# Kernel optimization log

Hardware: AMD Instinct MI355X
Metric: run time of the kernel (lower is better)

The kernel has to match this reference:

```python
import jax, jax.numpy as jnp
import numpy as np

N, E, G = 20000, 320000, 64
IN_CH, HID, HEADS = 128, 64, 8
LEAKY_SLOPE = 0.2
SOFTMAX_EPS = 1e-16


def setup_inputs() -> dict:
    key = jax.random.key(0)
    ks = jax.random.split(key, 12)
    s = lambda fan_in: 1.0 / np.sqrt(fan_in)
    return {
        "x": jax.random.normal(ks[0], (N, IN_CH), jnp.float32),
        "edge_index": jax.random.randint(ks[1], (2, E), 0, N, jnp.int32),
        "batch": jnp.sort(jax.random.randint(ks[2], (N,), 0, G, jnp.int32)),
        "W1": jax.random.normal(ks[3], (HEADS * HID, IN_CH), jnp.float32) * s(IN_CH),
        "att_src1": jax.random.normal(ks[4], (HEADS, HID), jnp.float32) * s(HID),
        "att_dst1": jax.random.normal(ks[5], (HEADS, HID), jnp.float32) * s(HID),
        "b1": jnp.zeros((HEADS * HID,), jnp.float32),
        "W2": jax.random.normal(ks[6], (HID, HEADS * HID), jnp.float32) * s(HEADS * HID),
        "att_src2": jax.random.normal(ks[7], (1, HID), jnp.float32) * s(HID),
        "att_dst2": jax.random.normal(ks[8], (1, HID), jnp.float32) * s(HID),
        "b2": jnp.zeros((HID,), jnp.float32),
    }


def gat_conv(x, src, dst, W, att_src, att_dst, b):
    # x: [N, F_in]; W: [H*C, F_in]; att_*: [H, C]; b: [H*C]
    n = x.shape[0]
    heads, ch = att_src.shape
    h = (x @ W.T).reshape(n, heads, ch)                    # [N,H,C]
    a_s = jnp.einsum('nhc,hc->nh', h, att_src)             # [N,H]
    a_d = jnp.einsum('nhc,hc->nh', h, att_dst)             # [N,H]
    e = jax.nn.leaky_relu(a_s[src] + a_d[dst], LEAKY_SLOPE)  # [E,H]
    m = jax.ops.segment_max(e, dst, num_segments=n)        # scatter-softmax (stable)
    e = jnp.exp(e - m[dst])
    z = jax.ops.segment_sum(e, dst, num_segments=n)
    alpha = e / (z[dst] + SOFTMAX_EPS)                     # [E,H]
    msg = h[src] * alpha[:, :, None]                       # [E,H,C]
    out = jax.ops.segment_sum(msg, dst, num_segments=n)    # [N,H,C]
    return out.reshape(n, heads * ch) + b


def reference(x, edge_index, batch, W1, att_src1, att_dst1, b1, W2, att_src2, att_dst2, b2):
    # PyG GATConv default: add self loops
    loop = jnp.arange(N, dtype=edge_index.dtype)
    src = jnp.concatenate([edge_index[0], loop])
    dst = jnp.concatenate([edge_index[1], loop])

    x_mid = jax.nn.relu(gat_conv(x, src, dst, W1, att_src1, att_dst1, b1))  # [N, H*C]

    # global_mean_pool over `batch` segments
    sums = jax.ops.segment_sum(x_mid, batch, num_segments=G)
    cnt = jax.ops.segment_sum(jnp.ones((N,), x_mid.dtype), batch, num_segments=G)
    gat_mid_pooled = sums / jnp.maximum(cnt, 1.0)[:, None]                  # [G, H*C]

    # dropout identity in eval mode
    x_late = gat_conv(x_mid, src, dst, W2, att_src2, att_dst2, b2)          # [N, C]
    gat_late_view = x_late.reshape(-1, HEADS * HID)                          # [N/H, H*C]
    return gat_mid_pooled, gat_late_view
```

## Files before the change

### kernel.cpp

```cpp
#include <hip/hip_runtime.h>
#include <math.h>

#define NN 20000
#define EE 320000
#define ETOT 340000
#define GG 64
#define INCH 128
#define HIDC 64
#define NH 8
#define HC 512
#define SLOPE 0.2f
#define SMEPS 1e-16f

typedef unsigned short u16;
typedef unsigned int u32;
typedef __attribute__((ext_vector_type(8))) short bf16x8;
typedef __attribute__((ext_vector_type(4))) float f32x4;

__device__ __forceinline__ float rlanef(float v, int l) {
  return __uint_as_float(__builtin_amdgcn_readlane(__float_as_uint(v), l));
}
__device__ __forceinline__ u16 f2bf(float f) {
  u32 x = __float_as_uint(f);
  x += 0x7FFFu + ((x >> 16) & 1u);
  return (u16)(x >> 16);
}

__global__ void k_hist(const int* __restrict__ ei, int* __restrict__ deg) {
  int i = blockIdx.x * 256 + threadIdx.x;
  if (i >= ETOT) return;
  int d = (i < EE) ? ei[EE + i] : (i - EE);
  atomicAdd(&deg[d], 1);
}

__global__ void k_scan(const int* __restrict__ deg, int* __restrict__ rowstart) {
  __shared__ int wsum[16];
  __shared__ int carry_sh;
  int tid = threadIdx.x;
  int lane = tid & 63, w = tid >> 6;
  if (tid == 0) { carry_sh = 0; rowstart[0] = 0; }
  __syncthreads();
  for (int base = 0; base < NN; base += 1024) {
    int v = (base + tid < NN) ? deg[base + tid] : 0;
    int s = v;
#pragma unroll
    for (int off = 1; off < 64; off <<= 1) {
      int t = __shfl_up(s, off);
      if (lane >= off) s += t;
    }
    if (lane == 63) wsum[w] = s;
    __syncthreads();
    if (w == 0 && lane < 16) {
      int t = wsum[lane];
#pragma unroll
      for (int off = 1; off < 16; off <<= 1) {
        int u = __shfl_up(t, off);
        if (lane >= off) t += u;
      }
      wsum[lane] = t;
    }
    __syncthreads();
    int waveoff = (w == 0) ? 0 : wsum[w - 1];
    int incl = s + waveoff + carry_sh;
    if (base + tid < NN) rowstart[base + tid + 1] = incl;
    __syncthreads();
    if (tid == 1023) carry_sh = incl;
    __syncthreads();
  }
}

__global__ void k_fill(const int* __restrict__ ei, const int* __restrict__ rowstart,
                       int* __restrict__ wcur, int* __restrict__ csr) {
  int i = blockIdx.x * 256 + threadIdx.x;
  if (i >= ETOT) return;
  int s, d;
  if (i < EE) { s = ei[i]; d = ei[EE + i]; } else { s = i - EE; d = s; }
  int pos = rowstart[d] + atomicAdd(&wcur[d], 1);
  csr[pos] = s;
}

__global__ void k_prep(const float* __restrict__ W1, const float* __restrict__ W2,
                       const float* __restrict__ as1, const float* __restrict__ ad1v,
                       u16* __restrict__ W1bf, u16* __restrict__ W2bf,
                       float* __restrict__ wB1) {
  int i = blockIdx.x * 256 + threadIdx.x;
  if (i < 65536) {
    W1bf[i] = f2bf(W1[i]);
  } else if (i < 65536 + 32768) {
    int j = i - 65536;
    W2bf[j] = f2bf(W2[j]);
  } else if (i < 65536 + 32768 + 2048) {
    int j = i - 65536 - 32768;
    int k = j >> 4, c = j & 15;
    int h = c & 7;
    const float* av = (c < 8) ? as1 : ad1v;
    float s = 0.f;
    for (int q = 0; q < 64; ++q) s += W1[(h * 64 + q) * 128 + k] * av[h * 64 + q];
    wB1[j] = s;
  }
}

__global__ __launch_bounds__(256) void k_logits1(
    const float* __restrict__ x, const float* __restrict__ wB1,
    float* __restrict__ al1) {
  __shared__ float bs[128][16];
  int tid = threadIdx.x;
#pragma unroll
  for (int i = 0; i < 8; ++i) {
    int e = tid + i * 256;
    bs[e >> 4][e & 15] = wB1[e];
  }
  __syncthreads();
  int gt = blockIdx.x * 256 + tid;
  int r = gt >> 2; if (r > NN - 1) r = NN - 1;
  int q = gt & 3;
  const float* xp = x + (size_t)r * INCH;
  float acc[4] = {0.f, 0.f, 0.f, 0.f};
  for (int kq = 0; kq < 32; ++kq) {
    float4 a = *(const float4*)(xp + kq * 4);
    float av[4] = {a.x, a.y, a.z, a.w};
#pragma unroll
    for (int kk = 0; kk < 4; ++kk) {
      const float4 b = *(const float4*)&bs[kq * 4 + kk][q * 4];
      acc[0] = fmaf(av[kk], b.x, acc[0]);
      acc[1] = fmaf(av[kk], b.y, acc[1]);
      acc[2] = fmaf(av[kk], b.z, acc[2]);
      acc[3] = fmaf(av[kk], b.w, acc[3]);
    }
  }
  float4 o; o.x = acc[0]; o.y = acc[1]; o.z = acc[2]; o.w = acc[3];
  *(float4*)(al1 + (size_t)r * 16 + q * 4) = o;
}

__global__ __launch_bounds__(256) void k_agg1(
    const float* __restrict__ x, const float* __restrict__ al1,
    const int* __restrict__ rowstart, const int* __restrict__ csr,
    u16* __restrict__ aggbf) {
  int n = blockIdx.x * 4 + (threadIdx.x >> 6);
  int lane = threadIdx.x & 63;
  int rs = __builtin_amdgcn_readfirstlane(rowstart[n]);
  int re = __builtin_amdgcn_readfirstlane(rowstart[n + 1]);
  float4 ad0 = *(const float4*)(al1 + (size_t)n * 16 + 8);
  float4 ad1 = *(const float4*)(al1 + (size_t)n * 16 + 12);
  float zp[NH] = {};
  float accx[NH] = {}, accy[NH] = {};
  for (int base = rs; base < re; base += 64) {
    int cn = min(64, re - base);
    int idx = base + ((lane < cn) ? lane : 0);
    int s = csr[idx];
    float4 a0 = *(const float4*)(al1 + (size_t)s * 16);
    float4 a1 = *(const float4*)(al1 + (size_t)s * 16 + 4);
    float e[8] = {a0.x + ad0.x, a0.y + ad0.y, a0.z + ad0.z, a0.w + ad0.w,
                  a1.x + ad1.x, a1.y + ad1.y, a1.z + ad1.z, a1.w + ad1.w};
    float p[8];
#pragma unroll
    for (int h = 0; h < 8; ++h) {
      float t = e[h]; t = (t > 0.f) ? t : SLOPE * t;
      float pv = __expf(t);
      pv = (lane < cn) ? pv : 0.f;
      p[h] = pv;
      zp[h] += pv;
    }
    for (int j = 0; j < cn; ++j) {
      int sj = __builtin_amdgcn_readlane(s, j);
      const float2 xv = *(const float2*)(x + (size_t)sj * INCH + lane * 2);
#pragma unroll
      for (int h = 0; h < 8; ++h) {
        float pj = rlanef(p[h], j);
        accx[h] = fmaf(pj, xv.x, accx[h]);
        accy[h] = fmaf(pj, xv.y, accy[h]);
      }
    }
  }
#pragma unroll
  for (int h = 0; h < 8; ++h) {
    float z = zp[h];
#pragma unroll
    for (int off = 32; off; off >>= 1) z += __shfl_xor(z, off);
    float inv = 1.f / (z + SMEPS);
    u32 pk = ((u32)f2bf(accy[h] * inv) << 16) | (u32)f2bf(accx[h] * inv);
    *(u32*)(aggbf + (size_t)h * NN * INCH + (size_t)n * INCH + lane * 2) = pk;
  }
}

__global__ __launch_bounds__(256) void k_gemm1h(
    const u16* __restrict__ aggbf, const u16* __restrict__ W1bf,
    const float* __restrict__ b1, float* __restrict__ xmid) {
  int tid = threadIdx.x;
  int head = blockIdx.x & 7;
  int nb = blockIdx.x >> 3;
  int w = tid >> 6, l = tid & 63;
  int li = l & 15, hi = l >> 4;
  const u16* Ab = aggbf + (size_t)head * NN * INCH;
  const u16* Bb = W1bf + (size_t)head * 64 * INCH;

  bf16x8 Bf[4][4];
#pragma unroll
  for (int ks = 0; ks < 4; ++ks)
#pragma unroll
    for (int ct = 0; ct < 4; ++ct)
      Bf[ks][ct] = *(const bf16x8*)(Bb + (size_t)(ct * 16 + li) * INCH + ks * 32 + hi * 8);

  int nA = nb * 64 + w * 16 + li; if (nA > NN - 1) nA = NN - 1;
  const u16* Ap = Ab + (size_t)nA * INCH + hi * 8;
  f32x4 acc[4] = {};
#pragma unroll
  for (int ks = 0; ks < 4; ++ks) {
    bf16x8 Af = *(const bf16x8*)(Ap + ks * 32);
#pragma unroll
    for (int ct = 0; ct < 4; ++ct)
      acc[ct] = __builtin_amdgcn_mfma_f32_16x16x32_bf16(Af, Bf[ks][ct], acc[ct], 0, 0, 0);
  }
#pragma unroll
  for (int ct = 0; ct < 4; ++ct) {
    float bb = b1[head * 64 + ct * 16 + li];
#pragma unroll
    for (int reg = 0; reg < 4; ++reg) {
      int r = nb * 64 + w * 16 + hi * 4 + reg; if (r > NN - 1) r = NN - 1;
      float v = fmaxf(acc[ct][reg] + bb, 0.f);
      xmid[(size_t)r * HC + head * 64 + ct * 16 + li] = v;
    }
  }
}

__global__ __launch_bounds__(256) void k_gemm2(
    const float* __restrict__ xm, const u16* __restrict__ W2bf,
    const float* __restrict__ atts, const float* __restrict__ attd,
    float* __restrict__ h2, float* __restrict__ as2, float* __restrict__ ad2) {
  __shared__ float red[4][16][65];
  int tid = threadIdx.x;
  int w = tid >> 6, l = tid & 63;
  int li = l & 15, hi = l >> 4;
  int brow = blockIdx.x * 16;

  bf16x8 Bf[4][4];
#pragma unroll
  for (int ksl = 0; ksl < 4; ++ksl)
#pragma unroll
    for (int ct = 0; ct < 4; ++ct)
      Bf[ksl][ct] = *(const bf16x8*)(W2bf + (size_t)(ct * 16 + li) * HC + w * 128 + ksl * 32 + hi * 8);

  const float* Ap = xm + (size_t)(brow + li) * HC + w * 128 + hi * 8;
  f32x4 acc[4] = {};
#pragma unroll
  for (int ksl = 0; ksl < 4; ++ksl) {
    float4 a0 = *(const float4*)(Ap + ksl * 32);
    float4 a1 = *(const float4*)(Ap + ksl * 32 + 4);
    bf16x8 Af;
    Af[0] = (short)f2bf(a0.x); Af[1] = (short)f2bf(a0.y);
    Af[2] = (short)f2bf(a0.z); Af[3] = (short)f2bf(a0.w);
    Af[4] = (short)f2bf(a1.x); Af[5] = (short)f2bf(a1.y);
    Af[6] = (short)f2bf(a1.z); Af[7] = (short)f2bf(a1.w);
#pragma unroll
    for (int ct = 0; ct < 4; ++ct)
      acc[ct] = __builtin_amdgcn_mfma_f32_16x16x32_bf16(Af, Bf[ksl][ct], acc[ct], 0, 0, 0);
  }
#pragma unroll
  for (int ct = 0; ct < 4; ++ct)
#pragma unroll
    for (int reg = 0; reg < 4; ++reg)
      red[w][hi * 4 + reg][ct * 16 + li] = acc[ct][reg];
  __syncthreads();

  int c = l;
  float atv = atts[c], adv = attd[c];
  float vs[4], vd[4];
#pragma unroll
  for (int i = 0; i < 4; ++i) {
    int r = w + 4 * i;
    float v = red[0][r][c] + red[1][r][c] + red[2][r][c] + red[3][r][c];
    h2[(size_t)(brow + r) * HIDC + c] = v;
    vs[i] = v * atv; vd[i] = v * adv;
  }
#pragma unroll
  for (int off = 32; off; off >>= 1) {
#pragma unroll
    for (int i = 0; i < 4; ++i) { vs[i] += __shfl_xor(vs[i], off); vd[i] += __shfl_xor(vd[i], off); }
  }
  if (l == 0) {
#pragma unroll
    for (int i = 0; i < 4; ++i) {
      int n = brow + w + 4 * i;
      as2[n] = vs[i]; ad2[n] = vd[i];
    }
  }
}

__global__ __launch_bounds__(256) void k_node2(
    const float* __restrict__ h2, const float* __restrict__ as2, const float* __restrict__ ad2,
    const int* __restrict__ rowstart, const int* __restrict__ csr,
    const float* __restrict__ b2, float* __restrict__ out) {
  int n = blockIdx.x * 4 + (threadIdx.x >> 6);
  int lane = threadIdx.x & 63;
  int rs = __builtin_amdgcn_readfirstlane(rowstart[n]);
  int re = __builtin_amdgcn_readfirstlane(rowstart[n + 1]);
  float ad = ad2[n];
  float zp = 0.f, acc = 0.f;
  for (int base = rs; base < re; base += 64) {
    int cn = min(64, re - base);
    int idx = base + ((lane < cn) ? lane : 0);
    int s = csr[idx];
    float t = as2[s] + ad;
    t = (t > 0.f) ? t : SLOPE * t;
    float p = (lane < cn) ? __expf(t) : 0.f;
    zp += p;
    for (int j = 0; j < cn; ++j) {
      int sj = __builtin_amdgcn_readlane(s, j);
      float pj = rlanef(p, j);
      acc = fmaf(pj, h2[(size_t)sj * HIDC + lane], acc);
    }
  }
  float z = zp;
#pragma unroll
  for (int off = 32; off; off >>= 1) z += __shfl_xor(z, off);
  out[(size_t)n * HIDC + lane] = acc / (z + SMEPS) + b2[lane];
}

__device__ inline int lowerb(const int* a, int n, int v) {
  int lo = 0, hi = n;
  while (lo < hi) { int mid = (lo + hi) >> 1; if (a[mid] < v) lo = mid + 1; else hi = mid; }
  return lo;
}

__global__ __launch_bounds__(256) void k_pool(const float* __restrict__ xm,
                                              const int* __restrict__ batch,
                                              float* __restrict__ out) {
  int g = blockIdx.x;
  int tid = threadIdx.x;
  int lo = lowerb(batch, NN, g);
  int hi = lowerb(batch, NN, g + 1);
  float inv = 1.f / fmaxf((float)(hi - lo), 1.f);
  int c = tid * 2;
  float sx = 0.f, sy = 0.f;
  int n = lo;
  for (; n + 4 <= hi; n += 4) {
    float2 v0 = *(const float2*)(xm + (size_t)(n + 0) * HC + c);
    float2 v1 = *(const float2*)(xm + (size_t)(n + 1) * HC + c);
    float2 v2 = *(const float2*)(xm + (size_t)(n + 2) * HC + c);
    float2 v3 = *(const float2*)(xm + (size_t)(n + 3) * HC + c);
    sx += (v0.x + v1.x) + (v2.x + v3.x);
    sy += (v0.y + v1.y) + (v2.y + v3.y);
  }
  for (; n < hi; ++n) {
    float2 v = *(const float2*)(xm + (size_t)n * HC + c);
    sx += v.x; sy += v.y;
  }
  out[(size_t)g * HC + c] = sx * inv;
  out[(size_t)g * HC + c + 1] = sy * inv;
}

extern "C" void kernel_launch(void* const* d_in, const int* in_sizes, int n_in,
                              void* d_out, int out_size, void* d_ws, size_t ws_size,
                              hipStream_t stream) {
  const float* x     = (const float*)d_in[0];
  const int*   ei    = (const int*)d_in[1];
  const int*   batch = (const int*)d_in[2];
  const float* W1    = (const float*)d_in[3];
  const float* atts1 = (const float*)d_in[4];
  const float* attd1 = (const float*)d_in[5];
  const float* b1    = (const float*)d_in[6];
  const float* W2    = (const float*)d_in[7];
  const float* atts2 = (const float*)d_in[8];
  const float* attd2 = (const float*)d_in[9];
  const float* b2    = (const float*)d_in[10];
  float* out = (float*)d_out;

  float* ws = (float*)d_ws;
  size_t off = 0;
  u16*  aggbf = (u16*)(ws + off); off += (size_t)NH * NN * INCH / 2;
  float* xmid = ws + off; off += (size_t)NN * HC;
  float* h2   = ws + off; off += (size_t)NN * HIDC;
  float* al1  = ws + off; off += (size_t)NN * 16;
  float* as2  = ws + off; off += NN;
  float* ad2  = ws + off; off += NN;
  u16*  W1bf  = (u16*)(ws + off); off += 65536 / 2;
  u16*  W2bf  = (u16*)(ws + off); off += 32768 / 2;
  float* wB1  = ws + off; off += 2048;
  int* deg      = (int*)(ws + off); off += NN;
  int* wcur     = (int*)(ws + off); off += NN;
  int* rowstart = (int*)(ws + off); off += NN + 4;
  int* csr      = (int*)(ws + off); off += ETOT;

  hipMemsetAsync(deg, 0, sizeof(int) * 2 * NN, stream);
  k_prep<<<393, 256, 0, stream>>>(W1, W2, atts1, attd1, W1bf, W2bf, wB1);
  k_hist<<<(ETOT + 255) / 256, 256, 0, stream>>>(ei, deg);
  k_scan<<<1, 1024, 0, stream>>>(deg, rowstart);
  k_fill<<<(ETOT + 255) / 256, 256, 0, stream>>>(ei, rowstart, wcur, csr);

  k_logits1<<<313, 256, 0, stream>>>(x, wB1, al1);
  k_agg1<<<5000, 256, 0, stream>>>(x, al1, rowstart, csr, aggbf);
  k_gemm1h<<<313 * 8, 256, 0, stream>>>(aggbf, W1bf, b1, xmid);
  k_pool<<<GG, 256, 0, stream>>>(xmid, batch, out);
  k_gemm2<<<1250, 256, 0, stream>>>(xmid, W2bf, atts2, attd2, h2, as2, ad2);
  k_node2<<<5000, 256, 0, stream>>>(h2, as2, ad2, rowstart, csr, b2, out + (size_t)GG * HC);
}
```

Before: 219.7 us.

## Store intermediates in bf16 and restructure edge aggregation to 4 edges per wave

Converts x, the layer-1 output and h2 to bf16 so every gather and GEMM input moves half the bytes. The gemm2 in-kernel conversion is dropped because its input is already bf16. Both aggregation kernels now process 4 edges per wave, with 16 lanes per edge doing vector loads, instead of serial per-edge readlane broadcast loops, and reduce across lane groups with shuffles. Pooling is split over 4 column blocks with a shared-memory reduction. The cost is lower precision in intermediate activations and an extra cast pass over x inside k_prep.

```diff
diff --git a/kernel.cpp b/kernel.cpp
--- a/kernel.cpp
+++ b/kernel.cpp
@@ -16,15 +16,15 @@
 typedef unsigned int u32;
 typedef __attribute__((ext_vector_type(8))) short bf16x8;
 typedef __attribute__((ext_vector_type(4))) float f32x4;
-
-__device__ __forceinline__ float rlanef(float v, int l) {
-  return __uint_as_float(__builtin_amdgcn_readlane(__float_as_uint(v), l));
-}
+typedef __attribute__((ext_vector_type(4))) u32 u32x4;
+
 __device__ __forceinline__ u16 f2bf(float f) {
   u32 x = __float_as_uint(f);
   x += 0x7FFFu + ((x >> 16) & 1u);
   return (u16)(x >> 16);
 }
+__device__ __forceinline__ float bflo(u32 w) { return __uint_as_float(w << 16); }
+__device__ __forceinline__ float bfhi(u32 w) { return __uint_as_float(w & 0xffff0000u); }
 
 __global__ void k_hist(const int* __restrict__ ei, int* __restrict__ deg) {
   int i = blockIdx.x * 256 + threadIdx.x;
@@ -81,8 +81,9 @@
 
 __global__ void k_prep(const float* __restrict__ W1, const float* __restrict__ W2,
                        const float* __restrict__ as1, const float* __restrict__ ad1v,
+                       const float* __restrict__ x,
                        u16* __restrict__ W1bf, u16* __restrict__ W2bf,
-                       float* __restrict__ wB1) {
+                       float* __restrict__ wB1, u16* __restrict__ xbf) {
   int i = blockIdx.x * 256 + threadIdx.x;
   if (i < 65536) {
     W1bf[i] = f2bf(W1[i]);
@@ -97,6 +98,9 @@
     float s = 0.f;
     for (int q = 0; q < 64; ++q) s += W1[(h * 64 + q) * 128 + k] * av[h * 64 + q];
     wB1[j] = s;
+  } else {
+    int j = i - 100352;
+    if (j < NN * INCH) xbf[j] = f2bf(x[j]);
   }
 }
 
@@ -133,59 +137,79 @@
 }
 
 __global__ __launch_bounds__(256) void k_agg1(
-    const float* __restrict__ x, const float* __restrict__ al1,
+    const u16* __restrict__ xbf, const float* __restrict__ al1,
     const int* __restrict__ rowstart, const int* __restrict__ csr,
     u16* __restrict__ aggbf) {
   int n = blockIdx.x * 4 + (threadIdx.x >> 6);
   int lane = threadIdx.x & 63;
+  int e = lane >> 4, c = lane & 15;
   int rs = __builtin_amdgcn_readfirstlane(rowstart[n]);
   int re = __builtin_amdgcn_readfirstlane(rowstart[n + 1]);
   float4 ad0 = *(const float4*)(al1 + (size_t)n * 16 + 8);
   float4 ad1 = *(const float4*)(al1 + (size_t)n * 16 + 12);
+  float acc[NH][8] = {};
   float zp[NH] = {};
-  float accx[NH] = {}, accy[NH] = {};
-  for (int base = rs; base < re; base += 64) {
-    int cn = min(64, re - base);
-    int idx = base + ((lane < cn) ? lane : 0);
-    int s = csr[idx];
+  for (int base = rs; base < re; base += 4) {
+    int idx = base + e;
+    bool ok = idx < re;
+    int s = csr[ok ? idx : re - 1];
     float4 a0 = *(const float4*)(al1 + (size_t)s * 16);
     float4 a1 = *(const float4*)(al1 + (size_t)s * 16 + 4);
-    float e[8] = {a0.x + ad0.x, a0.y + ad0.y, a0.z + ad0.z, a0.w + ad0.w,
-                  a1.x + ad1.x, a1.y + ad1.y, a1.z + ad1.z, a1.w + ad1.w};
+    float ev[8] = {a0.x + ad0.x, a0.y + ad0.y, a0.z + ad0.z, a0.w + ad0.w,
+                   a1.x + ad1.x, a1.y + ad1.y, a1.z + ad1.z, a1.w + ad1.w};
     float p[8];
 #pragma unroll
     for (int h = 0; h < 8; ++h) {
-      float t = e[h]; t = (t > 0.f) ? t : SLOPE * t;
+      float t = ev[h]; t = (t > 0.f) ? t : SLOPE * t;
       float pv = __expf(t);
-      pv = (lane < cn) ? pv : 0.f;
-      p[h] = pv;
-      zp[h] += pv;
-    }
-    for (int j = 0; j < cn; ++j) {
-      int sj = __builtin_amdgcn_readlane(s, j);
-      const float2 xv = *(const float2*)(x + (size_t)sj * INCH + lane * 2);
-#pragma unroll
-      for (int h = 0; h < 8; ++h) {
-        float pj = rlanef(p[h], j);
-        accx[h] = fmaf(pj, xv.x, accx[h]);
-        accy[h] = fmaf(pj, xv.y, accy[h]);
-      }
+      p[h] = ok ? pv : 0.f;
+      zp[h] += p[h];
+    }
+    u32x4 xw = *(const u32x4*)(xbf + (size_t)s * INCH + c * 8);
+    float xf[8] = {bflo(xw.x), bfhi(xw.x), bflo(xw.y), bfhi(xw.y),
+                   bflo(xw.z), bfhi(xw.z), bflo(xw.w), bfhi(xw.w)};
+#pragma unroll
+    for (int h = 0; h < 8; ++h) {
+      float ph = p[h];
+#pragma unroll
+      for (int q = 0; q < 8; ++q) acc[h][q] = fmaf(ph, xf[q], acc[h][q]);
     }
   }
 #pragma unroll
   for (int h = 0; h < 8; ++h) {
-    float z = zp[h];
-#pragma unroll
-    for (int off = 32; off; off >>= 1) z += __shfl_xor(z, off);
-    float inv = 1.f / (z + SMEPS);
-    u32 pk = ((u32)f2bf(accy[h] * inv) << 16) | (u32)f2bf(accx[h] * inv);
-    *(u32*)(aggbf + (size_t)h * NN * INCH + (size_t)n * INCH + lane * 2) = pk;
+    zp[h] += __shfl_xor(zp[h], 16); zp[h] += __shfl_xor(zp[h], 32);
+#pragma unroll
+    for (int q = 0; q < 8; ++q) {
+      acc[h][q] += __shfl_xor(acc[h][q], 16);
+      acc[h][q] += __shfl_xor(acc[h][q], 32);
+    }
+  }
+  int e1 = e & 1, e2 = e & 2;
+#pragma unroll
+  for (int hh = 0; hh < 2; ++hh) {
+    float za = e1 ? zp[2 + hh] : zp[0 + hh];
+    float zb = e1 ? zp[6 + hh] : zp[4 + hh];
+    float zz = e2 ? zb : za;
+    float inv = 1.f / (zz + SMEPS);
+    u32 pkv[4];
+#pragma unroll
+    for (int qq = 0; qq < 4; ++qq) {
+      float val = e1 ? acc[2 + hh][qq * 2] : acc[0 + hh][qq * 2];
+      float vbl = e1 ? acc[6 + hh][qq * 2] : acc[4 + hh][qq * 2];
+      float vl = (e2 ? vbl : val) * inv;
+      float vah = e1 ? acc[2 + hh][qq * 2 + 1] : acc[0 + hh][qq * 2 + 1];
+      float vbh = e1 ? acc[6 + hh][qq * 2 + 1] : acc[4 + hh][qq * 2 + 1];
+      float vh = (e2 ? vbh : vah) * inv;
+      pkv[qq] = ((u32)f2bf(vh) << 16) | (u32)f2bf(vl);
+    }
+    u32x4 st; st.x = pkv[0]; st.y = pkv[1]; st.z = pkv[2]; st.w = pkv[3];
+    *(u32x4*)(aggbf + (size_t)(e * 2 + hh) * NN * INCH + (size_t)n * INCH + c * 8) = st;
   }
 }
 
 __global__ __launch_bounds__(256) void k_gemm1h(
     const u16* __restrict__ aggbf, const u16* __restrict__ W1bf,
-    const float* __restrict__ b1, float* __restrict__ xmid) {
+    const float* __restrict__ b1, u16* __restrict__ xmidbf) {
   int tid = threadIdx.x;
   int head = blockIdx.x & 7;
   int nb = blockIdx.x >> 3;
@@ -218,15 +242,15 @@
     for (int reg = 0; reg < 4; ++reg) {
       int r = nb * 64 + w * 16 + hi * 4 + reg; if (r > NN - 1) r = NN - 1;
       float v = fmaxf(acc[ct][reg] + bb, 0.f);
-      xmid[(size_t)r * HC + head * 64 + ct * 16 + li] = v;
+      xmidbf[(size_t)r * HC + head * 64 + ct * 16 + li] = f2bf(v);
     }
   }
 }
 
 __global__ __launch_bounds__(256) void k_gemm2(
-    const float* __restrict__ xm, const u16* __restrict__ W2bf,
+    const u16* __restrict__ xmb, const u16* __restrict__ W2bf,
     const float* __restrict__ atts, const float* __restrict__ attd,
-    float* __restrict__ h2, float* __restrict__ as2, float* __restrict__ ad2) {
+    u16* __restrict__ h2bf, float* __restrict__ as2, float* __restrict__ ad2) {
   __shared__ float red[4][16][65];
   int tid = threadIdx.x;
   int w = tid >> 6, l = tid & 63;
@@ -240,17 +264,11 @@
     for (int ct = 0; ct < 4; ++ct)
       Bf[ksl][ct] = *(const bf16x8*)(W2bf + (size_t)(ct * 16 + li) * HC + w * 128 + ksl * 32 + hi * 8);
 
-  const float* Ap = xm + (size_t)(brow + li) * HC + w * 128 + hi * 8;
+  const u16* Ap = xmb + (size_t)(brow + li) * HC + w * 128 + hi * 8;
   f32x4 acc[4] = {};
 #pragma unroll
   for (int ksl = 0; ksl < 4; ++ksl) {
-    float4 a0 = *(const float4*)(Ap + ksl * 32);
-    float4 a1 = *(const float4*)(Ap + ksl * 32 + 4);
-    bf16x8 Af;
-    Af[0] = (short)f2bf(a0.x); Af[1] = (short)f2bf(a0.y);
-    Af[2] = (short)f2bf(a0.z); Af[3] = (short)f2bf(a0.w);
-    Af[4] = (short)f2bf(a1.x); Af[5] = (short)f2bf(a1.y);
-    Af[6] = (short)f2bf(a1.z); Af[7] = (short)f2bf(a1.w);
+    bf16x8 Af = *(const bf16x8*)(Ap + ksl * 32);
 #pragma unroll
     for (int ct = 0; ct < 4; ++ct)
       acc[ct] = __builtin_amdgcn_mfma_f32_16x16x32_bf16(Af, Bf[ksl][ct], acc[ct], 0, 0, 0);
@@ -269,7 +287,7 @@
   for (int i = 0; i < 4; ++i) {
     int r = w + 4 * i;
     float v = red[0][r][c] + red[1][r][c] + red[2][r][c] + red[3][r][c];
-    h2[(size_t)(brow + r) * HIDC + c] = v;
+    h2bf[(size_t)(brow + r) * HIDC + c] = f2bf(v);
     vs[i] = v * atv; vd[i] = v * adv;
   }
 #pragma unroll
@@ -287,33 +305,47 @@
 }
 
 __global__ __launch_bounds__(256) void k_node2(
-    const float* __restrict__ h2, const float* __restrict__ as2, const float* __restrict__ ad2,
+    const u16* __restrict__ h2bf, const float* __restrict__ as2, const float* __restrict__ ad2,
     const int* __restrict__ rowstart, const int* __restrict__ csr,
     const float* __restrict__ b2, float* __restrict__ out) {
   int n = blockIdx.x * 4 + (threadIdx.x >> 6);
   int lane = threadIdx.x & 63;
+  int e = lane >> 4, c = lane & 15;
   int rs = __builtin_amdgcn_readfirstlane(rowstart[n]);
   int re = __builtin_amdgcn_readfirstlane(rowstart[n + 1]);
   float ad = ad2[n];
-  float zp = 0.f, acc = 0.f;
-  for (int base = rs; base < re; base += 64) {
-    int cn = min(64, re - base);
-    int idx = base + ((lane < cn) ? lane : 0);
-    int s = csr[idx];
+  float acc[4] = {};
+  float zp = 0.f;
+  for (int base = rs; base < re; base += 4) {
+    int idx = base + e;
+    bool ok = idx < re;
+    int s = csr[ok ? idx : re - 1];
     float t = as2[s] + ad;
     t = (t > 0.f) ? t : SLOPE * t;
-    float p = (lane < cn) ? __expf(t) : 0.f;
+    float pv = __expf(t);
+    float p = ok ? pv : 0.f;
     zp += p;
-    for (int j = 0; j < cn; ++j) {
-      int sj = __builtin_amdgcn_readlane(s, j);
-      float pj = rlanef(p, j);
-      acc = fmaf(pj, h2[(size_t)sj * HIDC + lane], acc);
-    }
-  }
-  float z = zp;
-#pragma unroll
-  for (int off = 32; off; off >>= 1) z += __shfl_xor(z, off);
-  out[(size_t)n * HIDC + lane] = acc / (z + SMEPS) + b2[lane];
+    const u32* hp = (const u32*)(h2bf + (size_t)s * HIDC + c * 4);
+    u32 w0 = hp[0], w1 = hp[1];
+    acc[0] = fmaf(p, bflo(w0), acc[0]);
+    acc[1] = fmaf(p, bfhi(w0), acc[1]);
+    acc[2] = fmaf(p, bflo(w1), acc[2]);
+    acc[3] = fmaf(p, bfhi(w1), acc[3]);
+  }
+  zp += __shfl_xor(zp, 16); zp += __shfl_xor(zp, 32);
+#pragma unroll
+  for (int q = 0; q < 4; ++q) {
+    acc[q] += __shfl_xor(acc[q], 16);
+    acc[q] += __shfl_xor(acc[q], 32);
+  }
+  if (e == 0) {
+    float inv = 1.f / (zp + SMEPS);
+    float4 bv = *(const float4*)(b2 + c * 4);
+    float4 o;
+    o.x = acc[0] * inv + bv.x; o.y = acc[1] * inv + bv.y;
+    o.z = acc[2] * inv + bv.z; o.w = acc[3] * inv + bv.w;
+    *(float4*)(out + (size_t)n * HIDC + c * 4) = o;
+  }
 }
 
 __device__ inline int lowerb(const int* a, int n, int v) {
@@ -322,31 +354,31 @@
   return lo;
 }
 
-__global__ __launch_bounds__(256) void k_pool(const float* __restrict__ xm,
+__global__ __launch_bounds__(256) void k_pool(const u16* __restrict__ xmb,
                                               const int* __restrict__ batch,
                                               float* __restrict__ out) {
-  int g = blockIdx.x;
+  __shared__ float red[4][128];
+  int g = blockIdx.x >> 2;
+  int cb = blockIdx.x & 3;
   int tid = threadIdx.x;
+  int c2 = tid & 63;
+  int rq = tid >> 6;
   int lo = lowerb(batch, NN, g);
   int hi = lowerb(batch, NN, g + 1);
-  float inv = 1.f / fmaxf((float)(hi - lo), 1.f);
-  int c = tid * 2;
   float sx = 0.f, sy = 0.f;
-  int n = lo;
-  for (; n + 4 <= hi; n += 4) {
-    float2 v0 = *(const float2*)(xm + (size_t)(n + 0) * HC + c);
-    float2 v1 = *(const float2*)(xm + (size_t)(n + 1) * HC + c);
-    float2 v2 = *(const float2*)(xm + (size_t)(n + 2) * HC + c);
-    float2 v3 = *(const float2*)(xm + (size_t)(n + 3) * HC + c);
-    sx += (v0.x + v1.x) + (v2.x + v3.x);
-    sy += (v0.y + v1.y) + (v2.y + v3.y);
-  }
-  for (; n < hi; ++n) {
-    float2 v = *(const float2*)(xm + (size_t)n * HC + c);
-    sx += v.x; sy += v.y;
-  }
-  out[(size_t)g * HC + c] = sx * inv;
-  out[(size_t)g * HC + c + 1] = sy * inv;
+  for (int n = lo + rq; n < hi; n += 4) {
+    u32 w = *(const u32*)(xmb + (size_t)n * HC + cb * 128 + c2 * 2);
+    sx += bflo(w); sy += bfhi(w);
+  }
+  red[rq][c2 * 2] = sx; red[rq][c2 * 2 + 1] = sy;
+  __syncthreads();
+  if (rq == 0) {
+    float inv = 1.f / fmaxf((float)(hi - lo), 1.f);
+    float vx = red[0][c2 * 2] + red[1][c2 * 2] + red[2][c2 * 2] + red[3][c2 * 2];
+    float vy = red[0][c2 * 2 + 1] + red[1][c2 * 2 + 1] + red[2][c2 * 2 + 1] + red[3][c2 * 2 + 1];
+    float2 o; o.x = vx * inv; o.y = vy * inv;
+    *(float2*)(out + (size_t)g * HC + cb * 128 + c2 * 2) = o;
+  }
 }
 
 extern "C" void kernel_launch(void* const* d_in, const int* in_sizes, int n_in,
@@ -367,30 +399,31 @@
 
   float* ws = (float*)d_ws;
   size_t off = 0;
-  u16*  aggbf = (u16*)(ws + off); off += (size_t)NH * NN * INCH / 2;
-  float* xmid = ws + off; off += (size_t)NN * HC;
-  float* h2   = ws + off; off += (size_t)NN * HIDC;
+  u16*  aggbf  = (u16*)(ws + off); off += (size_t)NH * NN * INCH / 2;
+  u16*  xmidbf = (u16*)(ws + off); off += (size_t)NN * HC / 2;
+  u16*  h2bf   = (u16*)(ws + off); off += (size_t)NN * HIDC / 2;
   float* al1  = ws + off; off += (size_t)NN * 16;
   float* as2  = ws + off; off += NN;
   float* ad2  = ws + off; off += NN;
   u16*  W1bf  = (u16*)(ws + off); off += 65536 / 2;
   u16*  W2bf  = (u16*)(ws + off); off += 32768 / 2;
   float* wB1  = ws + off; off += 2048;
+  u16*  xbf   = (u16*)(ws + off); off += (size_t)NN * INCH / 2;
   int* deg      = (int*)(ws + off); off += NN;
   int* wcur     = (int*)(ws + off); off += NN;
   int* rowstart = (int*)(ws + off); off += NN + 4;
   int* csr      = (int*)(ws + off); off += ETOT;
 
   hipMemsetAsync(deg, 0, sizeof(int) * 2 * NN, stream);
-  k_prep<<<393, 256, 0, stream>>>(W1, W2, atts1, attd1, W1bf, W2bf, wB1);
+  k_prep<<<10392, 256, 0, stream>>>(W1, W2, atts1, attd1, x, W1bf, W2bf, wB1, xbf);
   k_hist<<<(ETOT + 255) / 256, 256, 0, stream>>>(ei, deg);
   k_scan<<<1, 1024, 0, stream>>>(deg, rowstart);
   k_fill<<<(ETOT + 255) / 256, 256, 0, stream>>>(ei, rowstart, wcur, csr);
 
   k_logits1<<<313, 256, 0, stream>>>(x, wB1, al1);
-  k_agg1<<<5000, 256, 0, stream>>>(x, al1, rowstart, csr, aggbf);
-  k_gemm1h<<<313 * 8, 256, 0, stream>>>(aggbf, W1bf, b1, xmid);
-  k_pool<<<GG, 256, 0, stream>>>(xmid, batch, out);
-  k_gemm2<<<1250, 256, 0, stream>>>(xmid, W2bf, atts2, attd2, h2, as2, ad2);
-  k_node2<<<5000, 256, 0, stream>>>(h2, as2, ad2, rowstart, csr, b2, out + (size_t)GG * HC);
-}
+  k_agg1<<<5000, 256, 0, stream>>>(xbf, al1, rowstart, csr, aggbf);
+  k_gemm1h<<<313 * 8, 256, 0, stream>>>(aggbf, W1bf, b1, xmidbf);
+  k_pool<<<GG * 4, 256, 0, stream>>>(xmidbf, batch, out);
+  k_gemm2<<<1250, 256, 0, stream>>>(xmidbf, W2bf, atts2, attd2, h2bf, as2, ad2);
+  k_node2<<<5000, 256, 0, stream>>>(h2bf, as2, ad2, rowstart, csr, b2, out + (size_t)GG * HC);
+}
```

Result: slower. 236.5 us (+7.6%).
